# Kernel optimization log

Hardware: AMD Instinct MI355X
Metric: run time of the kernel (lower is better)

## Reference

```python
import jax, jax.numpy as jnp
import numpy as np

NUM_HEADS = 16
ROPE_THETA = 10000.0


def _rope_tables(T, head_dim, dtype=jnp.float32):
    # Standard rotate-half RoPE tables: [T, head_dim]
    half = head_dim // 2
    inv_freq = 1.0 / (ROPE_THETA ** (jnp.arange(0, half, dtype=jnp.float32) / half))
    ang = jnp.arange(T, dtype=jnp.float32)[:, None] * inv_freq[None, :]  # [T, half]
    cos = jnp.concatenate([jnp.cos(ang), jnp.cos(ang)], axis=-1).astype(dtype)
    sin = jnp.concatenate([jnp.sin(ang), jnp.sin(ang)], axis=-1).astype(dtype)
    return cos, sin


def _apply_rope(x, cos, sin):
    # x: [B, T, H, D]; cos/sin: [T, D]
    D = x.shape[-1]
    x1, x2 = x[..., : D // 2], x[..., D // 2 :]
    rotated = jnp.concatenate([-x2, x1], axis=-1)
    return x * cos[None, :, None, :] + rotated * sin[None, :, None, :]


def setup_inputs() -> dict:
    key = jax.random.key(0)
    k1, k2, k3 = jax.random.split(key, 3)
    B, T, C = 4, 2048, 2048
    x = jax.random.normal(k1, (B, T, C), dtype=jnp.float32)
    w_attn = jax.random.normal(k2, (C, 3 * C), dtype=jnp.float32) * 0.02
    w_proj = jax.random.normal(k3, (C, C), dtype=jnp.float32) * 0.02
    return {"x": x, "w_attn": w_attn, "w_proj": w_proj}


def reference(x, w_attn, w_proj):
    B, T, C = x.shape
    H = NUM_HEADS
    D = C // H

    qkv = x @ w_attn                         # [B, T, 3C]
    q, k, v = jnp.split(qkv, 3, axis=-1)
    q = q.reshape(B, T, H, D)
    k = k.reshape(B, T, H, D)
    v = v.reshape(B, T, H, D)

    cos, sin = _rope_tables(T, D, x.dtype)
    q = _apply_rope(q, cos, sin)
    k = _apply_rope(k, cos, sin)

    # causal SDPA, heads-first layout [B, H, T, D]
    scale = 1.0 / jnp.sqrt(jnp.asarray(D, dtype=x.dtype))
    scores = jnp.einsum("bqhd,bkhd->bhqk", q, k) * scale  # [B, H, T, T]
    causal = jnp.tril(jnp.ones((T, T), dtype=bool))
    scores = jnp.where(causal[None, None], scores, jnp.finfo(scores.dtype).min)
    attn = jax.nn.softmax(scores, axis=-1)
    y = jnp.einsum("bhqk,bkhd->bqhd", attn, v).reshape(B, T, C)
    return y @ w_proj
```

## Files before the change

### kernel.cpp

```cpp
#include <hip/hip_runtime.h>

typedef __bf16 bf16;
typedef __bf16 bf16x8 __attribute__((ext_vector_type(8)));
typedef __bf16 bf16x4 __attribute__((ext_vector_type(4)));
typedef __bf16 bf16x2 __attribute__((ext_vector_type(2)));
typedef float floatx4 __attribute__((ext_vector_type(4)));
typedef float floatx16 __attribute__((ext_vector_type(16)));

#define NB 4
#define NT 2048
#define NC 2048
#define NH 16
#define ND 128
#define QKS 4096

__device__ __forceinline__ void load_lds16(const void* gptr, void* ldsptr) {
  __builtin_amdgcn_global_load_lds(
      (const __attribute__((address_space(1))) unsigned int*)gptr,
      (__attribute__((address_space(3))) unsigned int*)ldsptr, 16, 0, 0);
}

__device__ __forceinline__ unsigned pack2(float a, float b) {
  bf16x2 v;
  v[0] = (bf16)a; v[1] = (bf16)b;
  return __builtin_bit_cast(unsigned, v);
}

__global__ __launch_bounds__(256) void cast_f32_bf16(const float* __restrict__ in,
                                                     bf16* __restrict__ out) {
  const int i = blockIdx.x * 256 + threadIdx.x;
  const float4 v = ((const float4*)in)[i];
  bf16x4 o;
  o[0] = (bf16)v.x; o[1] = (bf16)v.y; o[2] = (bf16)v.z; o[3] = (bf16)v.w;
  ((bf16x4*)out)[i] = o;
}

__global__ __launch_bounds__(256) void transpose_cast(const float* __restrict__ in,
                                                      bf16* __restrict__ out,
                                                      int R, int Cc) {
  __shared__ float tile[128][65];
  const int r0 = blockIdx.y * 128, c0 = blockIdx.x * 64;
  const int rr = threadIdx.x >> 6, cc = threadIdx.x & 63;
#pragma unroll
  for (int i = 0; i < 32; ++i)
    tile[rr + i * 4][cc] = in[(size_t)(r0 + rr + i * 4) * Cc + c0 + cc];
  __syncthreads();
  const int rv = threadIdx.x & 63, halfr = (threadIdx.x >> 6) & 1, crh = threadIdx.x >> 7;
#pragma unroll
  for (int i = 0; i < 32; ++i) {
    const int cr = crh * 32 + i;
    out[(size_t)(c0 + cr) * R + r0 + halfr * 64 + rv] = (bf16)tile[halfr * 64 + rv][cr];
  }
}

__device__ __forceinline__ void stage_half(bf16* lds, const bf16* __restrict__ g,
                                           int row0, int k0, int h, int K,
                                           int w, int l) {
#pragma unroll
  for (int i = 0; i < 2; ++i) {
    const int fb = h * 1024 + w * 128 + i * 64;
    const int f = fb + l;
    const int r = f >> 3, cs = f & 7, c = cs ^ (r & 7);
    load_lds16(g + (size_t)(row0 + r) * K + k0 + c * 8, lds + fb * 8);
  }
}

template <int EPI, typename OutT>
__global__ __launch_bounds__(512, 2) void gemm_bt(const bf16* __restrict__ A,
                                                  const bf16* __restrict__ Bt,
                                                  OutT* __restrict__ C,
                                                  bf16* __restrict__ qk,
                                                  bf16* __restrict__ vt,
                                                  int M, int N, int K, int NTX) {
  __shared__ bf16 smem[65536];
  __shared__ float invf_s[64];
  const int tid = threadIdx.x;
  const int w = tid >> 6, l = tid & 63, quad = l >> 4, l16 = l & 15;
  const int wm = w >> 2, wn = w & 3;

  const int cpx = gridDim.x >> 3;
  const int orig = blockIdx.x;
  const int wgid = (orig & 7) * cpx + (orig >> 3);
  const int per = 8 * NTX;
  const int band = wgid / per, rem = wgid - band * per;
  const int by = band * 8 + (rem & 7), bx = rem >> 3;
  const int m0 = by * 256, n0 = bx * 256;

  if (EPI == 1 && tid < 64)
    invf_s[tid] = exp2f(-(float)tid * 0.20762050593046014f);

  const int KT = K >> 6;

  const floatx4 fzero = {0.f, 0.f, 0.f, 0.f};
  floatx4 acc[8][4];
#pragma unroll
  for (int i = 0; i < 8; ++i)
#pragma unroll
    for (int j = 0; j < 4; ++j) acc[i][j] = fzero;

  {
    bf16* As0 = smem;           bf16* Bs0 = smem + 16384;
    bf16* As1 = smem + 32768;
    stage_half(As0, A, m0, 0, 0, K, w, l);
    stage_half(As0, A, m0, 0, 1, K, w, l);
    stage_half(Bs0, Bt, n0, 0, 0, K, w, l);
    stage_half(Bs0, Bt, n0, 0, 1, K, w, l);
    if (KT > 1) {
      stage_half(As1, A, m0, 64, 0, K, w, l);
      stage_half(As1, A, m0, 64, 1, K, w, l);
      asm volatile("s_waitcnt vmcnt(4)" ::: "memory");
    } else {
      asm volatile("s_waitcnt vmcnt(0)" ::: "memory");
    }
    __builtin_amdgcn_sched_barrier(0);
    __builtin_amdgcn_s_barrier();
    __builtin_amdgcn_sched_barrier(0);
  }

#pragma unroll 1
  for (int t = 0; t < KT; ++t) {
    const int cur = t & 1;
    bf16* As_c = smem + cur * 32768;
    bf16* Bs_c = As_c + 16384;
    bf16* Bs_n = smem + (cur ^ 1) * 32768 + 16384;

    bf16x8 bfr[2][4];
#pragma unroll
    for (int p = 0; p < 4; ++p) {
      bf16x8 af[2][2];
#pragma unroll
      for (int mr = 0; mr < 2; ++mr)
#pragma unroll
        for (int ks = 0; ks < 2; ++ks) {
          const int row = wm * 128 + (p * 2 + mr) * 16 + l16;
          const int slot = (ks * 4 + quad) ^ (row & 7);
          af[mr][ks] = *(const bf16x8*)(As_c + row * 64 + slot * 8);
        }
      if (p == 0) {
#pragma unroll
        for (int ks = 0; ks < 2; ++ks)
#pragma unroll
          for (int ni = 0; ni < 4; ++ni) {
            const int row = wn * 64 + ni * 16 + l16;
            const int slot = (ks * 4 + quad) ^ (row & 7);
            bfr[ks][ni] = *(const bf16x8*)(Bs_c + row * 64 + slot * 8);
          }
      }
      if (p < 2 && t + 1 < KT)
        stage_half(Bs_n, Bt, n0, (t + 1) * 64, p, K, w, l);

      __builtin_amdgcn_s_barrier();
      asm volatile("s_waitcnt lgkmcnt(0)" ::: "memory");
      __builtin_amdgcn_sched_barrier(0);
      __builtin_amdgcn_s_setprio(1);
#pragma unroll
      for (int mr = 0; mr < 2; ++mr)
#pragma unroll
        for (int ks = 0; ks < 2; ++ks)
#pragma unroll
          for (int ni = 0; ni < 4; ++ni)
            acc[p * 2 + mr][ni] = __builtin_amdgcn_mfma_f32_16x16x32_bf16(
                af[mr][ks], bfr[ks][ni], acc[p * 2 + mr][ni], 0, 0, 0);
      __builtin_amdgcn_s_setprio(0);
      __builtin_amdgcn_s_barrier();
    }

    if (t + 1 < KT) {
      if (t + 2 < KT) {
        stage_half(As_c, A, m0, (t + 2) * 64, 0, K, w, l);
        stage_half(As_c, A, m0, (t + 2) * 64, 1, K, w, l);
        asm volatile("s_waitcnt vmcnt(4)" ::: "memory");
      } else {
        asm volatile("s_waitcnt vmcnt(0)" ::: "memory");
      }
      __builtin_amdgcn_sched_barrier(0);
      __builtin_amdgcn_s_barrier();
      __builtin_amdgcn_sched_barrier(0);
    }
  }

  if constexpr (EPI == 0) {
#pragma unroll
    for (int mi = 0; mi < 8; ++mi)
#pragma unroll
      for (int ni = 0; ni < 4; ++ni) {
        const int row = m0 + wm * 128 + mi * 16 + quad * 4;
        const int col = n0 + wn * 64 + ni * 16 + l16;
#pragma unroll
        for (int r = 0; r < 4; ++r)
          C[(size_t)(row + r) * N + col] = (OutT)acc[mi][ni][r];
      }
  } else {
    bf16* Tl = smem;
#pragma unroll 1
    for (int q = 0; q < 2; ++q) {
      if ((wn >> 1) == q) {
        bf16* Tg = Tl + wm * (128 * 130);
#pragma unroll
        for (int mi = 0; mi < 8; ++mi)
#pragma unroll
          for (int ni = 0; ni < 4; ++ni) {
            const int rl = mi * 16 + quad * 4;
            const int cl = (wn & 1) * 64 + ni * 16 + l16;
#pragma unroll
            for (int r = 0; r < 4; ++r)
              Tg[(rl + r) * 130 + cl] = (bf16)acc[mi][ni][r];
          }
      }
      __syncthreads();

      const int g = tid >> 8, t8 = tid & 255;
      const int m0q = m0 + g * 128, n0q = n0 + q * 128;
      bf16* Tq = Tl + g * (128 * 130);
      const int nt = n0q >> 7;
      if (nt < 32) {
        const int r = t8 >> 1, hd = t8 & 1;
        const float tt = (float)((m0q & (NT - 1)) + r);
        bf16* dst = qk + (size_t)(m0q + r) * QKS + n0q;
#pragma unroll
        for (int j8 = 0; j8 < 2; ++j8) {
          const int d0 = hd * 32 + j8 * 16;
          bf16x8 lo[2], hi[2];
#pragma unroll
          for (int half8 = 0; half8 < 2; ++half8) {
#pragma unroll
            for (int jj = 0; jj < 8; ++jj) {
              const int d = d0 + half8 * 8 + jj;
              const float x1 = (float)Tq[r * 130 + d];
              const float x2 = (float)Tq[r * 130 + d + 64];
              float s, c;
              __sincosf(tt * invf_s[d], &s, &c);
              lo[half8][jj] = (bf16)(x1 * c - x2 * s);
              hi[half8][jj] = (bf16)(x2 * c + x1 * s);
            }
            *(bf16x8*)(dst + d0 + half8 * 8) = lo[half8];
            *(bf16x8*)(dst + d0 + half8 * 8 + 64) = hi[half8];
          }
        }
      } else {
        const int h = nt - 32;
        const int b = m0q >> 11;
        const int t0 = m0q & (NT - 1);
        const int vbase = (b * NH + h) * ND;
#pragma unroll
        for (int ii = 0; ii < 8; ++ii) {
          const int dd = (t8 >> 4) + ii * 16;
          const int ch = t8 & 15;
          bf16x8 o;
#pragma unroll
          for (int j = 0; j < 8; ++j) o[j] = Tq[(ch * 8 + j) * 130 + dd];
          *(bf16x8*)(vt + (size_t)(vbase + dd) * NT + t0 + ch * 8) = o;
        }
      }
      __syncthreads();
    }
  }
}

__global__ __launch_bounds__(256) void attn_kernel(const bf16* __restrict__ qk,
                                                   const bf16* __restrict__ vt,
                                                   bf16* __restrict__ y) {
  __shared__ bf16 Ks[2][64 * 128];
  __shared__ bf16 Vs[2][128 * 64];

  const int pair = blockIdx.x, h = blockIdx.y, b = blockIdx.z;
  const int tid = threadIdx.x;
  const int w = tid >> 6, l = tid & 63, half = l >> 5, l32 = l & 31;
  const float SCL = 0.08838834764831845f * 1.4426950408889634f;

#pragma unroll 1
  for (int pi = 0; pi < 2; ++pi) {
    const int qt = pi ? (15 - pair) : pair;
    const int q0 = qt * 128;
    const int ntiles = qt * 2 + 2;
    const int qg = q0 + w * 32 + l32;

    bf16x8 aq[8];
#pragma unroll
    for (int ks = 0; ks < 8; ++ks)
      aq[ks] = *(const bf16x8*)(qk + (size_t)(b * NT + qg) * QKS + h * ND + ks * 16 + half * 8);

    floatx16 acc[4];
#pragma unroll
    for (int ni = 0; ni < 4; ++ni)
#pragma unroll
      for (int r = 0; r < 16; ++r) acc[ni][r] = 0.f;
    float mold = -3.0e38f, lsum = 0.f;

    {
#pragma unroll
      for (int i = 0; i < 4; ++i) {
        const int fb = i * 256 + w * 64, f = fb + l;
        { const int r = f >> 4, cs = f & 15, c = cs ^ (r & 15);
          load_lds16(qk + (size_t)(b * NT + r) * QKS + NC + h * ND + c * 8, &Ks[0][fb * 8]); }
        { const int r = f >> 3, cs = f & 7, c = cs ^ (r & 7);
          load_lds16(vt + ((size_t)((b * NH + h) * ND + r)) * NT + c * 8, &Vs[0][fb * 8]); }
      }
    }

#pragma unroll 1
    for (int it = 0; it < ntiles; ++it) {
      const int kv0 = it * 64;
      const int buf = it & 1;
      __syncthreads();

      if (it + 1 < ntiles) {
        const int kvn = kv0 + 64, nb = buf ^ 1;
#pragma unroll
        for (int i = 0; i < 4; ++i) {
          const int fb = i * 256 + w * 64, f = fb + l;
          { const int r = f >> 4, cs = f & 15, c = cs ^ (r & 15);
            load_lds16(qk + (size_t)(b * NT + kvn + r) * QKS + NC + h * ND + c * 8, &Ks[nb][fb * 8]); }
          { const int r = f >> 3, cs = f & 7, c = cs ^ (r & 7);
            load_lds16(vt + ((size_t)((b * NH + h) * ND + r)) * NT + kvn + c * 8, &Vs[nb][fb * 8]); }
        }
      }

      if (kv0 <= q0 + w * 32 + 31) {
        floatx16 st[2];
#pragma unroll
        for (int ki = 0; ki < 2; ++ki)
#pragma unroll
          for (int r = 0; r < 16; ++r) st[ki][r] = 0.f;
#pragma unroll
        for (int ks = 0; ks < 8; ++ks) {
          const int slot = (ks * 2 + half) ^ (l32 & 15);
#pragma unroll
          for (int ki = 0; ki < 2; ++ki) {
            const bf16x8 ak = *(const bf16x8*)(&Ks[buf][(ki * 32 + l32) * 128 + slot * 8]);
            st[ki] = __builtin_amdgcn_mfma_f32_32x32x16_bf16(ak, aq[ks], st[ki], 0, 0, 0);
          }
        }

        float mx = -3.0e38f;
        if (kv0 + 63 > q0 + w * 32) {
#pragma unroll
          for (int ki = 0; ki < 2; ++ki)
#pragma unroll
            for (int r = 0; r < 16; ++r) {
              const int kg = kv0 + ki * 32 + (r & 3) + 8 * (r >> 2) + 4 * half;
              float s = st[ki][r] * SCL;
              s = (kg > qg) ? -3.0e38f : s;
              st[ki][r] = s;
              mx = fmaxf(mx, s);
            }
        } else {
#pragma unroll
          for (int ki = 0; ki < 2; ++ki)
#pragma unroll
            for (int r = 0; r < 16; ++r) {
              const float s = st[ki][r] * SCL;
              st[ki][r] = s;
              mx = fmaxf(mx, s);
            }
        }
        mx = fmaxf(mx, __shfl_xor(mx, 32));

        const float mnew = fmaxf(mold, mx);
        const float al = exp2f(mold - mnew);
        float rs = 0.f;
#pragma unroll
        for (int ki = 0; ki < 2; ++ki)
#pragma unroll
          for (int r = 0; r < 16; ++r) {
            const float p = exp2f(st[ki][r] - mnew);
            st[ki][r] = p;
            rs += p;
          }
        rs += __shfl_xor(rs, 32);
        lsum = lsum * al + rs;
        mold = mnew;
#pragma unroll
        for (int ni = 0; ni < 4; ++ni)
#pragma unroll
          for (int r = 0; r < 16; ++r) acc[ni][r] *= al;

        unsigned pk[2][8];
#pragma unroll
        for (int ki = 0; ki < 2; ++ki)
#pragma unroll
          for (int d = 0; d < 8; ++d)
            pk[ki][d] = pack2(st[ki][2 * d], st[ki][2 * d + 1]);
        bf16x8 bp[4];
#pragma unroll
        for (int s = 0; s < 4; ++s) {
          const int ki = s >> 1, o = (s & 1) * 4;
          const unsigned a0 = pk[ki][o], a1 = pk[ki][o + 1], a2 = pk[ki][o + 2], a3 = pk[ki][o + 3];
          const unsigned s0 = (unsigned)__shfl_xor((int)a0, 32);
          const unsigned s1 = (unsigned)__shfl_xor((int)a1, 32);
          const unsigned s2 = (unsigned)__shfl_xor((int)a2, 32);
          const unsigned s3 = (unsigned)__shfl_xor((int)a3, 32);
          uint4 dw;
          dw.x = half ? s2 : a0;
          dw.y = half ? s3 : a1;
          dw.z = half ? a2 : s0;
          dw.w = half ? a3 : s1;
          bp[s] = __builtin_bit_cast(bf16x8, dw);
        }

#pragma unroll
        for (int ni = 0; ni < 4; ++ni) {
          const int rv = ni * 32 + l32;
#pragma unroll
          for (int s = 0; s < 4; ++s) {
            const int slot = (s * 2 + half) ^ (l32 & 7);
            const bf16x8 av = *(const bf16x8*)(&Vs[buf][rv * 64 + slot * 8]);
            acc[ni] = __builtin_amdgcn_mfma_f32_32x32x16_bf16(av, bp[s], acc[ni], 0, 0, 0);
          }
        }
      }
    }

    const float inv = 1.f / lsum;
    const size_t orow = (size_t)(b * NT + qg) * NC + h * ND;
#pragma unroll
    for (int ni = 0; ni < 4; ++ni)
#pragma unroll
      for (int rg = 0; rg < 4; ++rg) {
        bf16x4 o;
#pragma unroll
        for (int j = 0; j < 4; ++j) o[j] = (bf16)(acc[ni][rg * 4 + j] * inv);
        *(bf16x4*)(y + orow + ni * 32 + rg * 8 + half * 4) = o;
      }
    __syncthreads();
  }
}

extern "C" void kernel_launch(void* const* d_in, const int* in_sizes, int n_in,
                              void* d_out, int out_size, void* d_ws, size_t ws_size,
                              hipStream_t stream) {
  const float* x      = (const float*)d_in[0];
  const float* w_attn = (const float*)d_in[1];
  const float* w_proj = (const float*)d_in[2];
  float* out = (float*)d_out;
  char* ws = (char*)d_ws;

  bf16* qk  = (bf16*)(ws);
  bf16* vt  = (bf16*)(ws + 67108864);
  bf16* xb  = (bf16*)(ws + 100663296);
  bf16* wab = (bf16*)(ws + 134217728);
  bf16* y   = wab;
  bf16* wpb = (bf16*)(ws + 167772160);

  cast_f32_bf16<<<dim3(16384), dim3(256), 0, stream>>>(x, xb);
  transpose_cast<<<dim3(96, 16), dim3(256), 0, stream>>>(w_attn, wab, 2048, 6144);
  transpose_cast<<<dim3(32, 16), dim3(256), 0, stream>>>(w_proj, wpb, 2048, 2048);
  gemm_bt<1, float><<<dim3(768), dim3(512), 0, stream>>>(xb, wab, (float*)nullptr, qk, vt,
                                                         8192, 6144, 2048, 24);
  attn_kernel<<<dim3(8, 16, 4), dim3(256), 0, stream>>>(qk, vt, y);
  gemm_bt<0, float><<<dim3(256), dim3(512), 0, stream>>>(y, wpb, out, nullptr, nullptr,
                                                         8192, 2048, 2048, 8);
}
```

Baseline: 652.4 us.

## Restructure GEMM main loop with register double-buffered A fragments and simpler prefetch

Replaces the two-tile-ahead A prefetch with a one-tile-ahead scheme where both A and B for the next K tile are staged into the alternate LDS buffer during the current tile's compute. A fragments are now double-buffered in registers: the next 32-row slice is read from LDS while the current one feeds MFMAs, using partial lgkmcnt waits instead of a full drain. This aims to hide LDS read latency behind MFMA work and simplify the end-of-iteration sync. The cost is a shallower global prefetch distance, which may expose more global latency, plus extra fragment registers.

```diff
diff --git a/kernel.cpp b/kernel.cpp
--- a/kernel.cpp
+++ b/kernel.cpp
@@ -99,19 +99,13 @@
     for (int j = 0; j < 4; ++j) acc[i][j] = fzero;
 
   {
-    bf16* As0 = smem;           bf16* Bs0 = smem + 16384;
-    bf16* As1 = smem + 32768;
+    bf16* As0 = smem;
+    bf16* Bs0 = smem + 16384;
     stage_half(As0, A, m0, 0, 0, K, w, l);
     stage_half(As0, A, m0, 0, 1, K, w, l);
     stage_half(Bs0, Bt, n0, 0, 0, K, w, l);
     stage_half(Bs0, Bt, n0, 0, 1, K, w, l);
-    if (KT > 1) {
-      stage_half(As1, A, m0, 64, 0, K, w, l);
-      stage_half(As1, A, m0, 64, 1, K, w, l);
-      asm volatile("s_waitcnt vmcnt(4)" ::: "memory");
-    } else {
-      asm volatile("s_waitcnt vmcnt(0)" ::: "memory");
-    }
+    asm volatile("s_waitcnt vmcnt(0)" ::: "memory");
     __builtin_amdgcn_sched_barrier(0);
     __builtin_amdgcn_s_barrier();
     __builtin_amdgcn_sched_barrier(0);
@@ -122,21 +116,23 @@
     const int cur = t & 1;
     bf16* As_c = smem + cur * 32768;
     bf16* Bs_c = As_c + 16384;
-    bf16* Bs_n = smem + (cur ^ 1) * 32768 + 16384;
+    bf16* As_n = smem + (cur ^ 1) * 32768;
+    bf16* Bs_n = As_n + 16384;
 
     bf16x8 bfr[2][4];
+    bf16x8 af[2][2][2];
+
 #pragma unroll
     for (int p = 0; p < 4; ++p) {
-      bf16x8 af[2][2];
-#pragma unroll
-      for (int mr = 0; mr < 2; ++mr)
-#pragma unroll
-        for (int ks = 0; ks < 2; ++ks) {
-          const int row = wm * 128 + (p * 2 + mr) * 16 + l16;
-          const int slot = (ks * 4 + quad) ^ (row & 7);
-          af[mr][ks] = *(const bf16x8*)(As_c + row * 64 + slot * 8);
-        }
       if (p == 0) {
+#pragma unroll
+        for (int mr = 0; mr < 2; ++mr)
+#pragma unroll
+          for (int ks = 0; ks < 2; ++ks) {
+            const int row = wm * 128 + mr * 16 + l16;
+            const int slot = (ks * 4 + quad) ^ (row & 7);
+            af[0][mr][ks] = *(const bf16x8*)(As_c + row * 64 + slot * 8);
+          }
 #pragma unroll
         for (int ks = 0; ks < 2; ++ks)
 #pragma unroll
@@ -145,12 +141,40 @@
             const int slot = (ks * 4 + quad) ^ (row & 7);
             bfr[ks][ni] = *(const bf16x8*)(Bs_c + row * 64 + slot * 8);
           }
-      }
-      if (p < 2 && t + 1 < KT)
-        stage_half(Bs_n, Bt, n0, (t + 1) * 64, p, K, w, l);
-
+        __builtin_amdgcn_sched_barrier(0);
+#pragma unroll
+        for (int mr = 0; mr < 2; ++mr)
+#pragma unroll
+          for (int ks = 0; ks < 2; ++ks) {
+            const int row = wm * 128 + 32 + mr * 16 + l16;
+            const int slot = (ks * 4 + quad) ^ (row & 7);
+            af[1][mr][ks] = *(const bf16x8*)(As_c + row * 64 + slot * 8);
+          }
+        if (t + 1 < KT) {
+          stage_half(Bs_n, Bt, n0, (t + 1) * 64, 0, K, w, l);
+          stage_half(Bs_n, Bt, n0, (t + 1) * 64, 1, K, w, l);
+        }
+      } else if (p < 3) {
+#pragma unroll
+        for (int mr = 0; mr < 2; ++mr)
+#pragma unroll
+          for (int ks = 0; ks < 2; ++ks) {
+            const int row = wm * 128 + (p + 1) * 32 + mr * 16 + l16;
+            const int slot = (ks * 4 + quad) ^ (row & 7);
+            af[(p + 1) & 1][mr][ks] = *(const bf16x8*)(As_c + row * 64 + slot * 8);
+          }
+        if (p == 1 && t + 1 < KT) {
+          stage_half(As_n, A, m0, (t + 1) * 64, 0, K, w, l);
+          stage_half(As_n, A, m0, (t + 1) * 64, 1, K, w, l);
+        }
+      }
+
+      __builtin_amdgcn_sched_barrier(0);
       __builtin_amdgcn_s_barrier();
-      asm volatile("s_waitcnt lgkmcnt(0)" ::: "memory");
+      if (p < 3)
+        asm volatile("s_waitcnt lgkmcnt(4)" ::: "memory");
+      else
+        asm volatile("s_waitcnt lgkmcnt(0)" ::: "memory");
       __builtin_amdgcn_sched_barrier(0);
       __builtin_amdgcn_s_setprio(1);
 #pragma unroll
@@ -160,22 +184,13 @@
 #pragma unroll
           for (int ni = 0; ni < 4; ++ni)
             acc[p * 2 + mr][ni] = __builtin_amdgcn_mfma_f32_16x16x32_bf16(
-                af[mr][ks], bfr[ks][ni], acc[p * 2 + mr][ni], 0, 0, 0);
+                af[p & 1][mr][ks], bfr[ks][ni], acc[p * 2 + mr][ni], 0, 0, 0);
       __builtin_amdgcn_s_setprio(0);
+      if (p == 3) {
+        asm volatile("s_waitcnt vmcnt(0)" ::: "memory");
+        __builtin_amdgcn_sched_barrier(0);
+      }
       __builtin_amdgcn_s_barrier();
-    }
-
-    if (t + 1 < KT) {
-      if (t + 2 < KT) {
-        stage_half(As_c, A, m0, (t + 2) * 64, 0, K, w, l);
-        stage_half(As_c, A, m0, (t + 2) * 64, 1, K, w, l);
-        asm volatile("s_waitcnt vmcnt(4)" ::: "memory");
-      } else {
-        asm volatile("s_waitcnt vmcnt(0)" ::: "memory");
-      }
-      __builtin_amdgcn_sched_barrier(0);
-      __builtin_amdgcn_s_barrier();
-      __builtin_amdgcn_sched_barrier(0);
     }
   }
 
```

After: 632.1 us. 3.1% less time.

## Software-pipeline LDS fragment loads with register double-buffering in GEMM mainloop

Applied to the files above, without the earlier changes.

Restructures the GEMM K-loop so that A fragments for the next sub-tile are read from LDS into a second register buffer while the current MFMAs run. B fragments for the next K-tile are likewise prefetched at the end of each iteration. Global-to-LDS staging of the next tile now happens inside the p-loop, within the same iteration, instead of two tiles ahead. Row offsets are precomputed once to cut address arithmetic. This aims to hide LDS latency behind MFMA work, at the cost of more registers and a shallower global prefetch distance, since only one tile is now in flight.

```diff
diff --git a/kernel.cpp b/kernel.cpp
--- a/kernel.cpp
+++ b/kernel.cpp
@@ -91,6 +91,12 @@
 
   const int KT = K >> 6;
 
+  const int sw = l16 & 7;
+  const int aoff0 = (wm * 128 + l16) * 64 + ((0 + quad) ^ sw) * 8;
+  const int aoff1 = (wm * 128 + l16) * 64 + ((4 + quad) ^ sw) * 8;
+  const int boff0 = (wn * 64 + l16) * 64 + ((0 + quad) ^ sw) * 8;
+  const int boff1 = (wn * 64 + l16) * 64 + ((4 + quad) ^ sw) * 8;
+
   const floatx4 fzero = {0.f, 0.f, 0.f, 0.f};
   floatx4 acc[8][4];
 #pragma unroll
@@ -98,60 +104,75 @@
 #pragma unroll
     for (int j = 0; j < 4; ++j) acc[i][j] = fzero;
 
+  bf16x8 af[2][2][2];
+  bf16x8 bfr[2][4];
+
   {
-    bf16* As0 = smem;           bf16* Bs0 = smem + 16384;
-    bf16* As1 = smem + 32768;
-    stage_half(As0, A, m0, 0, 0, K, w, l);
-    stage_half(As0, A, m0, 0, 1, K, w, l);
-    stage_half(Bs0, Bt, n0, 0, 0, K, w, l);
-    stage_half(Bs0, Bt, n0, 0, 1, K, w, l);
-    if (KT > 1) {
-      stage_half(As1, A, m0, 64, 0, K, w, l);
-      stage_half(As1, A, m0, 64, 1, K, w, l);
-      asm volatile("s_waitcnt vmcnt(4)" ::: "memory");
-    } else {
-      asm volatile("s_waitcnt vmcnt(0)" ::: "memory");
-    }
+    stage_half(smem, A, m0, 0, 0, K, w, l);
+    stage_half(smem, A, m0, 0, 1, K, w, l);
+    stage_half(smem + 16384, Bt, n0, 0, 0, K, w, l);
+    stage_half(smem + 16384, Bt, n0, 0, 1, K, w, l);
+    asm volatile("s_waitcnt vmcnt(0)" ::: "memory");
     __builtin_amdgcn_sched_barrier(0);
     __builtin_amdgcn_s_barrier();
     __builtin_amdgcn_sched_barrier(0);
+#pragma unroll
+    for (int mr = 0; mr < 2; ++mr) {
+      af[0][mr][0] = *(const bf16x8*)(smem + aoff0 + mr * 1024);
+      af[0][mr][1] = *(const bf16x8*)(smem + aoff1 + mr * 1024);
+    }
+#pragma unroll
+    for (int ni = 0; ni < 4; ++ni) {
+      bfr[0][ni] = *(const bf16x8*)(smem + 16384 + boff0 + ni * 1024);
+      bfr[1][ni] = *(const bf16x8*)(smem + 16384 + boff1 + ni * 1024);
+    }
   }
 
 #pragma unroll 1
   for (int t = 0; t < KT; ++t) {
-    const int cur = t & 1;
-    bf16* As_c = smem + cur * 32768;
-    bf16* Bs_c = As_c + 16384;
-    bf16* Bs_n = smem + (cur ^ 1) * 32768 + 16384;
-
-    bf16x8 bfr[2][4];
+    bf16* cur = smem + ((t & 1) << 15);
+    bf16* nxt = smem + (((t + 1) & 1) << 15);
+
 #pragma unroll
     for (int p = 0; p < 4; ++p) {
-      bf16x8 af[2][2];
-#pragma unroll
-      for (int mr = 0; mr < 2; ++mr)
-#pragma unroll
-        for (int ks = 0; ks < 2; ++ks) {
-          const int row = wm * 128 + (p * 2 + mr) * 16 + l16;
-          const int slot = (ks * 4 + quad) ^ (row & 7);
-          af[mr][ks] = *(const bf16x8*)(As_c + row * 64 + slot * 8);
-        }
-      if (p == 0) {
-#pragma unroll
-        for (int ks = 0; ks < 2; ++ks)
-#pragma unroll
-          for (int ni = 0; ni < 4; ++ni) {
-            const int row = wn * 64 + ni * 16 + l16;
-            const int slot = (ks * 4 + quad) ^ (row & 7);
-            bfr[ks][ni] = *(const bf16x8*)(Bs_c + row * 64 + slot * 8);
-          }
-      }
-      if (p < 2 && t + 1 < KT)
-        stage_half(Bs_n, Bt, n0, (t + 1) * 64, p, K, w, l);
-
-      __builtin_amdgcn_s_barrier();
-      asm volatile("s_waitcnt lgkmcnt(0)" ::: "memory");
-      __builtin_amdgcn_sched_barrier(0);
+      if (p < 3) {
+#pragma unroll
+        for (int mr = 0; mr < 2; ++mr) {
+          af[(p + 1) & 1][mr][0] =
+              *(const bf16x8*)(cur + aoff0 + ((p + 1) * 32 + mr * 16) * 64);
+          af[(p + 1) & 1][mr][1] =
+              *(const bf16x8*)(cur + aoff1 + ((p + 1) * 32 + mr * 16) * 64);
+        }
+        if (p == 0 && t + 1 < KT) {
+          stage_half(nxt + 16384, Bt, n0, (t + 1) * 64, 0, K, w, l);
+          stage_half(nxt + 16384, Bt, n0, (t + 1) * 64, 1, K, w, l);
+        }
+        if (p == 1 && t + 1 < KT) {
+          stage_half(nxt, A, m0, (t + 1) * 64, 0, K, w, l);
+          stage_half(nxt, A, m0, (t + 1) * 64, 1, K, w, l);
+        }
+        __builtin_amdgcn_sched_barrier(0);
+        __builtin_amdgcn_s_barrier();
+        asm volatile("s_waitcnt lgkmcnt(4)" ::: "memory");
+        __builtin_amdgcn_sched_barrier(0);
+      } else {
+        asm volatile("s_waitcnt vmcnt(0)" ::: "memory");
+        __builtin_amdgcn_sched_barrier(0);
+        __builtin_amdgcn_s_barrier();
+        __builtin_amdgcn_sched_barrier(0);
+        if (t + 1 < KT) {
+#pragma unroll
+          for (int mr = 0; mr < 2; ++mr) {
+            af[0][mr][0] = *(const bf16x8*)(nxt + aoff0 + mr * 1024);
+            af[0][mr][1] = *(const bf16x8*)(nxt + aoff1 + mr * 1024);
+          }
+          asm volatile("s_waitcnt lgkmcnt(4)" ::: "memory");
+        } else {
+          asm volatile("s_waitcnt lgkmcnt(0)" ::: "memory");
+        }
+        __builtin_amdgcn_sched_barrier(0);
+      }
+
       __builtin_amdgcn_s_setprio(1);
 #pragma unroll
       for (int mr = 0; mr < 2; ++mr)
@@ -160,22 +181,19 @@
 #pragma unroll
           for (int ni = 0; ni < 4; ++ni)
             acc[p * 2 + mr][ni] = __builtin_amdgcn_mfma_f32_16x16x32_bf16(
-                af[mr][ks], bfr[ks][ni], acc[p * 2 + mr][ni], 0, 0, 0);
+                af[p & 1][mr][ks], bfr[ks][ni], acc[p * 2 + mr][ni], 0, 0, 0);
       __builtin_amdgcn_s_setprio(0);
+      __builtin_amdgcn_sched_barrier(0);
+
+      if (p == 3 && t + 1 < KT) {
+#pragma unroll
+        for (int ni = 0; ni < 4; ++ni) {
+          bfr[0][ni] = *(const bf16x8*)(nxt + 16384 + boff0 + ni * 1024);
+          bfr[1][ni] = *(const bf16x8*)(nxt + 16384 + boff1 + ni * 1024);
+        }
+        __builtin_amdgcn_sched_barrier(0);
+      }
       __builtin_amdgcn_s_barrier();
-    }
-
-    if (t + 1 < KT) {
-      if (t + 2 < KT) {
-        stage_half(As_c, A, m0, (t + 2) * 64, 0, K, w, l);
-        stage_half(As_c, A, m0, (t + 2) * 64, 1, K, w, l);
-        asm volatile("s_waitcnt vmcnt(4)" ::: "memory");
-      } else {
-        asm volatile("s_waitcnt vmcnt(0)" ::: "memory");
-      }
-      __builtin_amdgcn_sched_barrier(0);
-      __builtin_amdgcn_s_barrier();
-      __builtin_amdgcn_sched_barrier(0);
     }
   }
 
```

After: 631.3 us. -3.2%, faster.
